# Kernel tuning notes

Hardware: AMD Instinct MI355X
Metric: run time of the kernel (lower is better)

The kernel has to match this reference:

```python
import jax, jax.numpy as jnp
import numpy as np

B, F, C, NS, P, N = 256, 2048, 16384, 65536, 8, 32
T, W_BU, W_H, P_MARGIN, N_MARGIN = 1.0, 1.0, 10.0, 0.1, 0.1


def setup_inputs() -> dict:
    key = jax.random.key(0)
    ks = jax.random.split(key, 8)
    inputs = jax.random.normal(ks[0], (B, F), jnp.float32)
    targets = jax.random.randint(ks[1], (B,), 0, C)
    # batch global indices: unique (original .item() assumes a single match)
    indexs = jax.random.permutation(ks[2], NS)[:B].astype(jnp.int64) if False else jax.random.permutation(ks[2], jnp.arange(NS))[:B]
    # positive candidates drawn from in-batch indices so they are found in `indexs`
    pos_sel = jax.random.randint(ks[3], (B, P), 0, B)
    ppairs = indexs[pos_sel]
    # negative candidates: arbitrary global indices (mostly not in batch)
    npairs = jax.random.randint(ks[4], (B, N), 0, NS)
    all_label_to_clusterid = jax.random.randint(ks[5], (NS,), 0, C)
    V = jax.random.normal(ks[6], (C, F), jnp.float32)
    V = V / jnp.linalg.norm(V, axis=1, keepdims=True)  # bank rows are L2-normalized by the update rule
    return {"inputs": inputs, "targets": targets, "ppairs": ppairs, "npairs": npairs,
            "indexs": indexs, "all_label_to_clusterid": all_label_to_clusterid, "V": V, "epoch": 1}


def _forward(inputs, targets, ppairs, npairs, indexs, all_label_to_clusterid, V, epoch):
    # Exclusive branch: logits against the memory bank (V treated as constant)
    outputs = (inputs @ V.T) * T  # [B, C]
    logp = jax.nn.log_softmax(outputs, axis=1)
    bu_loss = -jnp.mean(jnp.take_along_axis(logp, targets[:, None], axis=1))

    # ms_loss (use_prior=True, use_table=True)
    ni = inputs / jnp.linalg.norm(inputs, axis=1, keepdims=True)
    sims = ni @ ni.T          # [B, B]
    tsims = ni @ V.T          # [B, C]

    # positives found in the batch: (ppair == indexs).nonzero()
    mp = ppairs[:, :, None] == indexs[None, None, :]        # [B, P, B]
    found_p = jnp.any(mp, axis=2)
    idx_p = jnp.argmax(mp, axis=2)
    psim_b = jnp.take_along_axis(sims, idx_p, axis=1)       # [B, P]
    mask_pb = found_p & (ppairs >= 0)
    # table positive: tsims[i, target] appended if nonzero
    tp = jnp.take_along_axis(tsims, targets[:, None], axis=1)  # [B, 1]
    mask_tp = tp != 0
    psims = jnp.concatenate([psim_b, tp], axis=1)           # [B, P+1]
    pmask = jnp.concatenate([mask_pb, mask_tp], axis=1)

    # negatives found in the batch
    mn = npairs[:, :, None] == indexs[None, None, :]        # [B, N, B]
    found_n = jnp.any(mn, axis=2)
    idx_n = jnp.argmax(mn, axis=2)
    nsim_b = jnp.take_along_axis(sims, idx_n, axis=1)       # [B, N]
    mask_nb = found_n & (npairs >= 0)
    # table negative appended for EVERY npair (indent level in original): tsims[i, clusterid[npair]]
    ncid = all_label_to_clusterid[jnp.clip(npairs, 0, None)]
    tn = jnp.take_along_axis(tsims, ncid, axis=1)           # [B, N]
    mask_tn = (npairs >= 0) & (tn != 0)
    nsims = jnp.concatenate([nsim_b, tn], axis=1)           # [B, 2N]
    nmask = jnp.concatenate([mask_nb, mask_tn], axis=1)

    # thresholds: max(nsims) or -3 (+p_margin); min(psims) or 3 (-n_margin)
    p_thrd = jnp.where(jnp.any(nmask, 1), jnp.max(jnp.where(nmask, nsims, -jnp.inf), 1), -3.0) + P_MARGIN
    n_thrd = jnp.where(jnp.any(pmask, 1), jnp.min(jnp.where(pmask, psims, jnp.inf), 1), 3.0) - N_MARGIN

    hp = pmask & (psims < p_thrd[:, None])
    hn = nmask & (nsims > n_thrd[:, None]) & (nsims < 0.999999)

    hp_sum = jnp.sum(jnp.where(hp, jnp.exp(-2.0 * (psims - 0.5)), 0.0))
    hn_sum = jnp.sum(jnp.where(hn, jnp.exp(50.0 * (nsims - 0.5)), 0.0))
    hp_loss = jnp.where(jnp.any(hp), 0.5 * jnp.log1p(hp_sum), 0.0)
    hn_loss = jnp.where(jnp.any(hn), (1.0 / 50.0) * jnp.log1p(hn_sum), 0.0)
    # original builds hpsims/hnsims with torch.tensor(...), which DETACHES them
    h_loss = jax.lax.stop_gradient(hp_loss + hn_loss)

    loss = W_BU * bu_loss + W_H * h_loss
    return loss, outputs


def reference(inputs, targets, ppairs, npairs, indexs, all_label_to_clusterid, V, epoch):
    return _forward(inputs, targets, ppairs, npairs, indexs, all_label_to_clusterid, V, epoch)
```

## Files before the change

kernel.cpp:

```cpp
#include <hip/hip_runtime.h>
#include <hip/hip_bf16.h>
#include <math.h>

#define B_SZ 256
#define F_SZ 2048
#define C_SZ 16384
#define P_SZ 8
#define N_SZ 32
#define NTILE 256

typedef __bf16 bf16x8 __attribute__((ext_vector_type(8)));
typedef float f32x4 __attribute__((ext_vector_type(4)));
typedef unsigned short us8 __attribute__((ext_vector_type(8)));

typedef __attribute__((address_space(3))) unsigned int lds_u32;
typedef __attribute__((address_space(1))) const unsigned int glb_u32;

__device__ __forceinline__ unsigned short f2bf(float x) {
    union { float f; unsigned int u; } v; v.f = x;
    unsigned int r = v.u + 0x7FFFu + ((v.u >> 16) & 1u);
    return (unsigned short)(r >> 16);
}

__global__ __launch_bounds__(256) void prep_kernel(const float* __restrict__ inputs,
                                                   unsigned short* __restrict__ Abf,
                                                   float* __restrict__ norms) {
    const int row = blockIdx.x;
    const int tid = threadIdx.x;
    const float* rp = inputs + (size_t)row * F_SZ + tid * 8;
    float4 v0 = *(const float4*)(rp);
    float4 v1 = *(const float4*)(rp + 4);
    us8 o;
    o[0]=f2bf(v0.x); o[1]=f2bf(v0.y); o[2]=f2bf(v0.z); o[3]=f2bf(v0.w);
    o[4]=f2bf(v1.x); o[5]=f2bf(v1.y); o[6]=f2bf(v1.z); o[7]=f2bf(v1.w);
    *(us8*)(Abf + (size_t)row * F_SZ + tid * 8) = o;
    float ss = v0.x*v0.x + v0.y*v0.y + v0.z*v0.z + v0.w*v0.w
             + v1.x*v1.x + v1.y*v1.y + v1.z*v1.z + v1.w*v1.w;
    __shared__ float red[256];
    red[tid] = ss; __syncthreads();
    for (int s = 128; s > 0; s >>= 1) { if (tid < s) red[tid] += red[tid+s]; __syncthreads(); }
    if (tid == 0) norms[row] = sqrtf(red[0]);
}

#define BM 128
#define BN 64
#define BK 64
#define BPAD 72
#define KITERS (F_SZ / BK)

__global__ __launch_bounds__(256) void gemm_kernel(const unsigned short* __restrict__ Abf,
                                                   const float* __restrict__ V,
                                                   float* __restrict__ Cout,
                                                   float* __restrict__ pmax,
                                                   float* __restrict__ psum) {
    __shared__ unsigned short As[2][BM * BK];
    __shared__ unsigned short Bs[2][BN * BPAD];

    const int tid = threadIdx.x;
    const int lane = tid & 63;
    const int wid = tid >> 6;
    const int q = lane >> 4, l16 = lane & 15;
    const int bm0 = blockIdx.y * BM;
    const int bn0 = blockIdx.x * BN;

    f32x4 acc[2][4];
    #pragma unroll
    for (int i = 0; i < 2; i++)
        #pragma unroll
        for (int j = 0; j < 4; j++) acc[i][j] = (f32x4){0.f, 0.f, 0.f, 0.f};

    const int arow = tid >> 3;
    const int cfetch = (tid & 7) ^ (arow & 7);
    const unsigned short* AgBase = Abf + (size_t)(bm0 + arow) * F_SZ + cfetch * 8;

    const int brow = tid >> 2, bseg = tid & 3;
    const float* BgBase = V + (size_t)(bn0 + brow) * F_SZ + bseg * 16;
    unsigned short* Bsd0 = &Bs[0][brow * BPAD + bseg * 16];
    unsigned short* Bsd1 = &Bs[1][brow * BPAD + bseg * 16];

    float4 b0, b1, b2, b3;

    auto issueA = [&](int buf, int k0) {
        #pragma unroll
        for (int j = 0; j < 4; j++) {
            __builtin_amdgcn_global_load_lds(
                (glb_u32*)(AgBase + (size_t)j * 32 * F_SZ + k0),
                (lds_u32*)&As[buf][(size_t)(j * 256 + wid * 64) * 8],
                16, 0, 0);
        }
    };
    auto loadB = [&](int k0) {
        b0 = *(const float4*)(BgBase + k0);
        b1 = *(const float4*)(BgBase + k0 + 4);
        b2 = *(const float4*)(BgBase + k0 + 8);
        b3 = *(const float4*)(BgBase + k0 + 12);
    };
    auto writeB = [&](unsigned short* dst) {
        us8 w0, w1;
        w0[0]=f2bf(b0.x); w0[1]=f2bf(b0.y); w0[2]=f2bf(b0.z); w0[3]=f2bf(b0.w);
        w0[4]=f2bf(b1.x); w0[5]=f2bf(b1.y); w0[6]=f2bf(b1.z); w0[7]=f2bf(b1.w);
        w1[0]=f2bf(b2.x); w1[1]=f2bf(b2.y); w1[2]=f2bf(b2.z); w1[3]=f2bf(b2.w);
        w1[4]=f2bf(b3.x); w1[5]=f2bf(b3.y); w1[6]=f2bf(b3.z); w1[7]=f2bf(b3.w);
        *(us8*)dst = w0;
        *(us8*)(dst + 8) = w1;
    };

    issueA(0, 0);
    loadB(0);
    writeB(Bsd0);
    __syncthreads();

    for (int it = 0; it < KITERS; ++it) {
        const int cur = it & 1;
        const bool more = (it + 1) < KITERS;
        if (more) {
            issueA(cur ^ 1, (it + 1) * BK);
            loadB((it + 1) * BK);
        }
        #pragma unroll
        for (int ks = 0; ks < 2; ++ks) {
            bf16x8 af[2], bfv[4];
            #pragma unroll
            for (int mi = 0; mi < 2; ++mi) {
                const int row = wid * 32 + mi * 16 + l16;
                const int kc = ks * 4 + q;
                af[mi] = *(const bf16x8*)&As[cur][(size_t)(row * 8 + (kc ^ (row & 7))) * 8];
            }
            #pragma unroll
            for (int ni = 0; ni < 4; ++ni)
                bfv[ni] = *(const bf16x8*)&Bs[cur][(ni * 16 + l16) * BPAD + ks * 32 + q * 8];
            #pragma unroll
            for (int mi = 0; mi < 2; ++mi)
                #pragma unroll
                for (int ni = 0; ni < 4; ++ni)
                    acc[mi][ni] = __builtin_amdgcn_mfma_f32_16x16x32_bf16(af[mi], bfv[ni], acc[mi][ni], 0, 0, 0);
        }
        if (more) writeB(cur ? Bsd0 : Bsd1);
        __syncthreads();
    }

    #pragma unroll
    for (int mi = 0; mi < 2; ++mi) {
        const int r0 = bm0 + wid * 32 + mi * 16 + q * 4;
        #pragma unroll
        for (int ni = 0; ni < 4; ++ni) {
            const int c0 = bn0 + ni * 16 + l16;
            #pragma unroll
            for (int r = 0; r < 4; ++r)
                Cout[(size_t)(r0 + r) * C_SZ + c0] = acc[mi][ni][r];
        }
    }

    const int tileIdx = blockIdx.x;
    #pragma unroll
    for (int mi = 0; mi < 2; ++mi) {
        #pragma unroll
        for (int r = 0; r < 4; ++r) {
            float mloc = fmaxf(fmaxf(acc[mi][0][r], acc[mi][1][r]),
                               fmaxf(acc[mi][2][r], acc[mi][3][r]));
            #pragma unroll
            for (int off = 1; off < 16; off <<= 1)
                mloc = fmaxf(mloc, __shfl_xor(mloc, off, 64));
            float sloc = __expf(acc[mi][0][r] - mloc) + __expf(acc[mi][1][r] - mloc)
                       + __expf(acc[mi][2][r] - mloc) + __expf(acc[mi][3][r] - mloc);
            #pragma unroll
            for (int off = 1; off < 16; off <<= 1)
                sloc += __shfl_xor(sloc, off, 64);
            if (l16 == 0) {
                const int grow = bm0 + wid * 32 + mi * 16 + q * 4 + r;
                pmax[grow * NTILE + tileIdx] = mloc;
                psum[grow * NTILE + tileIdx] = sloc;
            }
        }
    }
}

__global__ __launch_bounds__(256) void softmax_combine_kernel(
    const float* __restrict__ pmax, const float* __restrict__ psum,
    const float* __restrict__ outputs, const int* __restrict__ targets,
    float* __restrict__ bu_part)
{
    const int row = blockIdx.x;
    const int tid = threadIdx.x;
    __shared__ float rm[256], rs[256];
    rm[tid] = pmax[row * NTILE + tid];
    rs[tid] = psum[row * NTILE + tid];
    __syncthreads();
    for (int s = 128; s > 0; s >>= 1) {
        if (tid < s) {
            float m1 = rm[tid], s1 = rs[tid];
            float m2 = rm[tid + s], s2 = rs[tid + s];
            float nm = fmaxf(m1, m2);
            rs[tid] = s1 * __expf(m1 - nm) + s2 * __expf(m2 - nm);
            rm[tid] = nm;
        }
        __syncthreads();
    }
    if (tid == 0) {
        float logZ = rm[0] + logf(rs[0]);
        bu_part[row] = -(outputs[(size_t)row * C_SZ + targets[row]] - logZ);
    }
}

__global__ __launch_bounds__(256) void pairs_kernel(
    const float* __restrict__ inputs, const int* __restrict__ targets,
    const int* __restrict__ ppairs, const int* __restrict__ npairs,
    const int* __restrict__ indexs, const int* __restrict__ cluster,
    const float* __restrict__ outputs, const float* __restrict__ norms,
    float* __restrict__ hp_part, float* __restrict__ hn_part,
    int* __restrict__ flag_part)
{
    const int i = blockIdx.x;
    const int tid = threadIdx.x;
    __shared__ int idxbuf[B_SZ];
    __shared__ int pj[P_SZ];
    __shared__ int nj[N_SZ];
    __shared__ float simp[P_SZ];
    __shared__ float simn[N_SZ];
    __shared__ float tnv[N_SZ];
    __shared__ float s_tp;

    idxbuf[tid] = indexs[tid];
    __syncthreads();

    const float* row = outputs + (size_t)i * C_SZ;
    const float ni_norm = norms[i];

    if (tid < P_SZ) {
        int pp = ppairs[i * P_SZ + tid];
        int f = -1;
        if (pp >= 0) for (int j = 0; j < B_SZ; j++) if (idxbuf[j] == pp) { f = j; break; }
        pj[tid] = f;
    } else if (tid < P_SZ + N_SZ) {
        int t = tid - P_SZ;
        int np = npairs[i * N_SZ + t];
        int f = -1;
        if (np >= 0) for (int j = 0; j < B_SZ; j++) if (idxbuf[j] == np) { f = j; break; }
        nj[t] = f;
        int cid = cluster[np < 0 ? 0 : np];
        tnv[t] = row[cid] / ni_norm;
    }
    if (tid == P_SZ + N_SZ) s_tp = row[targets[i]] / ni_norm;
    __syncthreads();

    const int lane = tid & 63, wv = tid >> 6;
    for (int qq = wv; qq < P_SZ + N_SZ; qq += 4) {
        int j = (qq < P_SZ) ? pj[qq] : nj[qq - P_SZ];
        float s = 0.f;
        if (j >= 0) {
            const float* xi = inputs + (size_t)i * F_SZ;
            const float* xj = inputs + (size_t)j * F_SZ;
            float d = 0.f;
            for (int k = lane; k < F_SZ; k += 64) d += xi[k] * xj[k];
            for (int off = 32; off > 0; off >>= 1) d += __shfl_down(d, off);
            s = d / (ni_norm * norms[j]);
        }
        if (lane == 0) { if (qq < P_SZ) simp[qq] = s; else simn[qq - P_SZ] = s; }
    }
    __syncthreads();

    if (tid == 0) {
        float psims[P_SZ + 1]; bool pmask[P_SZ + 1];
        for (int p = 0; p < P_SZ; p++) {
            int pp = ppairs[i * P_SZ + p];
            pmask[p] = (pj[p] >= 0) && (pp >= 0);
            psims[p] = simp[p];
        }
        psims[P_SZ] = s_tp; pmask[P_SZ] = (s_tp != 0.0f);

        float nsims[2 * N_SZ]; bool nmask[2 * N_SZ];
        for (int t = 0; t < N_SZ; t++) {
            int np = npairs[i * N_SZ + t];
            nmask[t] = (nj[t] >= 0) && (np >= 0);
            nsims[t] = simn[t];
            nsims[N_SZ + t] = tnv[t];
            nmask[N_SZ + t] = (np >= 0) && (tnv[t] != 0.0f);
        }
        bool anyp = false, anyn = false;
        float maxn = -INFINITY, minp = INFINITY;
        for (int t = 0; t < 2 * N_SZ; t++) if (nmask[t]) { anyn = true; maxn = fmaxf(maxn, nsims[t]); }
        for (int p = 0; p < P_SZ + 1; p++) if (pmask[p]) { anyp = true; minp = fminf(minp, psims[p]); }
        float p_thrd = (anyn ? maxn : -3.0f) + 0.1f;
        float n_thrd = (anyp ? minp : 3.0f) - 0.1f;
        float hps = 0.f, hns = 0.f; int fl = 0;
        for (int p = 0; p < P_SZ + 1; p++)
            if (pmask[p] && psims[p] < p_thrd) { fl |= 1; hps += expf(-2.0f * (psims[p] - 0.5f)); }
        for (int t = 0; t < 2 * N_SZ; t++)
            if (nmask[t] && nsims[t] > n_thrd && nsims[t] < 0.999999f) { fl |= 2; hns += expf(50.0f * (nsims[t] - 0.5f)); }
        hp_part[i] = hps; hn_part[i] = hns; flag_part[i] = fl;
    }
}

__global__ __launch_bounds__(256) void finalize_kernel(
    const float* __restrict__ bu_part, const float* __restrict__ hp_part,
    const float* __restrict__ hn_part, const int* __restrict__ flag_part,
    float* __restrict__ d_out)
{
    __shared__ float r1[256], r2[256], r3[256];
    __shared__ int rf[256];
    const int tid = threadIdx.x;
    r1[tid] = bu_part[tid]; r2[tid] = hp_part[tid]; r3[tid] = hn_part[tid]; rf[tid] = flag_part[tid];
    __syncthreads();
    for (int s = 128; s > 0; s >>= 1) {
        if (tid < s) { r1[tid] += r1[tid+s]; r2[tid] += r2[tid+s]; r3[tid] += r3[tid+s]; rf[tid] |= rf[tid+s]; }
        __syncthreads();
    }
    if (tid == 0) {
        float bu = r1[0] / (float)B_SZ;
        float hp_loss = (rf[0] & 1) ? 0.5f * log1pf(r2[0]) : 0.0f;
        float hn_loss = (rf[0] & 2) ? (1.0f / 50.0f) * log1pf(r3[0]) : 0.0f;
        d_out[0] = 1.0f * bu + 10.0f * (hp_loss + hn_loss);
    }
}

extern "C" void kernel_launch(void* const* d_in, const int* in_sizes, int n_in,
                              void* d_out, int out_size, void* d_ws, size_t ws_size,
                              hipStream_t stream) {
    const float* inputs  = (const float*)d_in[0];
    const int*   targets = (const int*)d_in[1];
    const int*   ppairs  = (const int*)d_in[2];
    const int*   npairs  = (const int*)d_in[3];
    const int*   indexs  = (const int*)d_in[4];
    const int*   cluster = (const int*)d_in[5];
    const float* V       = (const float*)d_in[6];
    float* out = (float*)d_out;

    char* ws = (char*)d_ws;
    unsigned short* Abf = (unsigned short*)ws;
    float* norms   = (float*)(ws + (size_t)B_SZ * F_SZ * 2);
    float* bu_part = norms + B_SZ;
    float* hp_part = bu_part + B_SZ;
    float* hn_part = hp_part + B_SZ;
    int*   flag_part = (int*)(hn_part + B_SZ);
    float* pmax = (float*)(flag_part + B_SZ);
    float* psum = pmax + (size_t)B_SZ * NTILE;

    prep_kernel<<<B_SZ, 256, 0, stream>>>(inputs, Abf, norms);
    gemm_kernel<<<dim3(C_SZ / BN, B_SZ / BM), 256, 0, stream>>>(Abf, V, out + 1, pmax, psum);
    softmax_combine_kernel<<<B_SZ, 256, 0, stream>>>(pmax, psum, out + 1, targets, bu_part);
    pairs_kernel<<<B_SZ, 256, 0, stream>>>(inputs, targets, ppairs, npairs, indexs,
                                           cluster, out + 1, norms,
                                           hp_part, hn_part, flag_part);
    finalize_kernel<<<1, 256, 0, stream>>>(bu_part, hp_part, hn_part, flag_part, out);
}
```

Measured before the change: 302.8 us.

## Cover all batch rows per block so each V tile is read once

The GEMM now uses 1024-thread blocks spanning all 256 batch rows with a 64-column slice of V. Each V element is therefore loaded and converted to bf16 once instead of once per row-block. K-step drops to 32 and each wave computes a 32x32 sub-tile, with partial softmax stats emitted per 32-column half (512 tiles). The combine kernel reduces two entries per thread. The trade-off is more barriers per unit of MFMA work and fewer blocks in the grid, which lowers latency hiding.

```diff
diff --git a/kernel.cpp b/kernel.cpp
--- a/kernel.cpp
+++ b/kernel.cpp
@@ -7,11 +7,12 @@
 #define C_SZ 16384
 #define P_SZ 8
 #define N_SZ 32
-#define NTILE 256
+#define NTILE 512
 
 typedef __bf16 bf16x8 __attribute__((ext_vector_type(8)));
 typedef float f32x4 __attribute__((ext_vector_type(4)));
 typedef unsigned short us8 __attribute__((ext_vector_type(8)));
+typedef unsigned short us4 __attribute__((ext_vector_type(4)));
 
 typedef __attribute__((address_space(3))) unsigned int lds_u32;
 typedef __attribute__((address_space(1))) const unsigned int glb_u32;
@@ -42,67 +43,56 @@
     if (tid == 0) norms[row] = sqrtf(red[0]);
 }
 
-#define BM 128
+#define BM 256
 #define BN 64
-#define BK 64
-#define BPAD 72
+#define BK 32
+#define BPAD 40
 #define KITERS (F_SZ / BK)
 
-__global__ __launch_bounds__(256) void gemm_kernel(const unsigned short* __restrict__ Abf,
-                                                   const float* __restrict__ V,
-                                                   float* __restrict__ Cout,
-                                                   float* __restrict__ pmax,
-                                                   float* __restrict__ psum) {
-    __shared__ unsigned short As[2][BM * BK];
+__global__ __launch_bounds__(1024) void gemm_kernel(const unsigned short* __restrict__ Abf,
+                                                    const float* __restrict__ V,
+                                                    float* __restrict__ Cout,
+                                                    float* __restrict__ pmax,
+                                                    float* __restrict__ psum) {
+    __shared__ unsigned short As[2][4 * 256 * 8];
     __shared__ unsigned short Bs[2][BN * BPAD];
 
     const int tid = threadIdx.x;
     const int lane = tid & 63;
     const int wid = tid >> 6;
+    const int wrow = wid & 7, wcol = wid >> 3;
     const int q = lane >> 4, l16 = lane & 15;
-    const int bm0 = blockIdx.y * BM;
     const int bn0 = blockIdx.x * BN;
 
-    f32x4 acc[2][4];
+    f32x4 acc[2][2];
     #pragma unroll
     for (int i = 0; i < 2; i++)
         #pragma unroll
-        for (int j = 0; j < 4; j++) acc[i][j] = (f32x4){0.f, 0.f, 0.f, 0.f};
-
-    const int arow = tid >> 3;
-    const int cfetch = (tid & 7) ^ (arow & 7);
-    const unsigned short* AgBase = Abf + (size_t)(bm0 + arow) * F_SZ + cfetch * 8;
-
-    const int brow = tid >> 2, bseg = tid & 3;
-    const float* BgBase = V + (size_t)(bn0 + brow) * F_SZ + bseg * 16;
-    unsigned short* Bsd0 = &Bs[0][brow * BPAD + bseg * 16];
-    unsigned short* Bsd1 = &Bs[1][brow * BPAD + bseg * 16];
-
-    float4 b0, b1, b2, b3;
+        for (int j = 0; j < 2; j++) acc[i][j] = (f32x4){0.f, 0.f, 0.f, 0.f};
+
+    const int arow = tid & 255, achk = tid >> 8;
+    const unsigned short* AgBase = Abf + (size_t)arow * F_SZ + achk * 8;
+
+    const int brow = tid >> 3, bseg = tid & 7;
+    const float* BgBase = V + (size_t)(bn0 + brow) * F_SZ + bseg * 4;
+    unsigned short* Bsd0 = &Bs[0][brow * BPAD + bseg * 4];
+    unsigned short* Bsd1 = &Bs[1][brow * BPAD + bseg * 4];
+
+    float4 bv;
 
     auto issueA = [&](int buf, int k0) {
-        #pragma unroll
-        for (int j = 0; j < 4; j++) {
-            __builtin_amdgcn_global_load_lds(
-                (glb_u32*)(AgBase + (size_t)j * 32 * F_SZ + k0),
-                (lds_u32*)&As[buf][(size_t)(j * 256 + wid * 64) * 8],
-                16, 0, 0);
-        }
+        __builtin_amdgcn_global_load_lds((glb_u32*)(AgBase + k0),
+                                         (lds_u32*)&As[buf][(size_t)tid * 8], 16, 0, 0);
     };
     auto loadB = [&](int k0) {
-        b0 = *(const float4*)(BgBase + k0);
-        b1 = *(const float4*)(BgBase + k0 + 4);
-        b2 = *(const float4*)(BgBase + k0 + 8);
-        b3 = *(const float4*)(BgBase + k0 + 12);
+        if (tid < 512) bv = *(const float4*)(BgBase + k0);
     };
     auto writeB = [&](unsigned short* dst) {
-        us8 w0, w1;
-        w0[0]=f2bf(b0.x); w0[1]=f2bf(b0.y); w0[2]=f2bf(b0.z); w0[3]=f2bf(b0.w);
-        w0[4]=f2bf(b1.x); w0[5]=f2bf(b1.y); w0[6]=f2bf(b1.z); w0[7]=f2bf(b1.w);
-        w1[0]=f2bf(b2.x); w1[1]=f2bf(b2.y); w1[2]=f2bf(b2.z); w1[3]=f2bf(b2.w);
-        w1[4]=f2bf(b3.x); w1[5]=f2bf(b3.y); w1[6]=f2bf(b3.z); w1[7]=f2bf(b3.w);
-        *(us8*)dst = w0;
-        *(us8*)(dst + 8) = w1;
+        if (tid < 512) {
+            us4 w;
+            w[0]=f2bf(bv.x); w[1]=f2bf(bv.y); w[2]=f2bf(bv.z); w[3]=f2bf(bv.w);
+            *(us4*)dst = w;
+        }
     };
 
     issueA(0, 0);
@@ -117,57 +107,53 @@
             issueA(cur ^ 1, (it + 1) * BK);
             loadB((it + 1) * BK);
         }
-        #pragma unroll
-        for (int ks = 0; ks < 2; ++ks) {
-            bf16x8 af[2], bfv[4];
+        bf16x8 af[2], bfv[2];
+        #pragma unroll
+        for (int mi = 0; mi < 2; ++mi) {
+            const int row = wrow * 32 + mi * 16 + l16;
+            af[mi] = *(const bf16x8*)&As[cur][(size_t)(q * 256 + row) * 8];
+        }
+        #pragma unroll
+        for (int ni = 0; ni < 2; ++ni) {
+            const int col = wcol * 32 + ni * 16 + l16;
+            bfv[ni] = *(const bf16x8*)&Bs[cur][col * BPAD + q * 8];
+        }
+        #pragma unroll
+        for (int mi = 0; mi < 2; ++mi)
             #pragma unroll
-            for (int mi = 0; mi < 2; ++mi) {
-                const int row = wid * 32 + mi * 16 + l16;
-                const int kc = ks * 4 + q;
-                af[mi] = *(const bf16x8*)&As[cur][(size_t)(row * 8 + (kc ^ (row & 7))) * 8];
-            }
-            #pragma unroll
-            for (int ni = 0; ni < 4; ++ni)
-                bfv[ni] = *(const bf16x8*)&Bs[cur][(ni * 16 + l16) * BPAD + ks * 32 + q * 8];
-            #pragma unroll
-            for (int mi = 0; mi < 2; ++mi)
-                #pragma unroll
-                for (int ni = 0; ni < 4; ++ni)
-                    acc[mi][ni] = __builtin_amdgcn_mfma_f32_16x16x32_bf16(af[mi], bfv[ni], acc[mi][ni], 0, 0, 0);
-        }
+            for (int ni = 0; ni < 2; ++ni)
+                acc[mi][ni] = __builtin_amdgcn_mfma_f32_16x16x32_bf16(af[mi], bfv[ni], acc[mi][ni], 0, 0, 0);
         if (more) writeB(cur ? Bsd0 : Bsd1);
         __syncthreads();
     }
 
     #pragma unroll
     for (int mi = 0; mi < 2; ++mi) {
-        const int r0 = bm0 + wid * 32 + mi * 16 + q * 4;
-        #pragma unroll
-        for (int ni = 0; ni < 4; ++ni) {
-            const int c0 = bn0 + ni * 16 + l16;
+        const int r0 = wrow * 32 + mi * 16 + q * 4;
+        #pragma unroll
+        for (int ni = 0; ni < 2; ++ni) {
+            const int c0 = bn0 + wcol * 32 + ni * 16 + l16;
             #pragma unroll
             for (int r = 0; r < 4; ++r)
                 Cout[(size_t)(r0 + r) * C_SZ + c0] = acc[mi][ni][r];
         }
     }
 
-    const int tileIdx = blockIdx.x;
+    const int tileIdx = blockIdx.x * 2 + wcol;
     #pragma unroll
     for (int mi = 0; mi < 2; ++mi) {
         #pragma unroll
         for (int r = 0; r < 4; ++r) {
-            float mloc = fmaxf(fmaxf(acc[mi][0][r], acc[mi][1][r]),
-                               fmaxf(acc[mi][2][r], acc[mi][3][r]));
+            float mloc = fmaxf(acc[mi][0][r], acc[mi][1][r]);
             #pragma unroll
             for (int off = 1; off < 16; off <<= 1)
                 mloc = fmaxf(mloc, __shfl_xor(mloc, off, 64));
-            float sloc = __expf(acc[mi][0][r] - mloc) + __expf(acc[mi][1][r] - mloc)
-                       + __expf(acc[mi][2][r] - mloc) + __expf(acc[mi][3][r] - mloc);
+            float sloc = __expf(acc[mi][0][r] - mloc) + __expf(acc[mi][1][r] - mloc);
             #pragma unroll
             for (int off = 1; off < 16; off <<= 1)
                 sloc += __shfl_xor(sloc, off, 64);
             if (l16 == 0) {
-                const int grow = bm0 + wid * 32 + mi * 16 + q * 4 + r;
+                const int grow = wrow * 32 + mi * 16 + q * 4 + r;
                 pmax[grow * NTILE + tileIdx] = mloc;
                 psum[grow * NTILE + tileIdx] = sloc;
             }
@@ -183,16 +169,19 @@
     const int row = blockIdx.x;
     const int tid = threadIdx.x;
     __shared__ float rm[256], rs[256];
-    rm[tid] = pmax[row * NTILE + tid];
-    rs[tid] = psum[row * NTILE + tid];
+    float m1 = pmax[row * NTILE + tid],       s1 = psum[row * NTILE + tid];
+    float m2 = pmax[row * NTILE + tid + 256], s2 = psum[row * NTILE + tid + 256];
+    float nm = fmaxf(m1, m2);
+    rm[tid] = nm;
+    rs[tid] = s1 * __expf(m1 - nm) + s2 * __expf(m2 - nm);
     __syncthreads();
     for (int s = 128; s > 0; s >>= 1) {
         if (tid < s) {
-            float m1 = rm[tid], s1 = rs[tid];
-            float m2 = rm[tid + s], s2 = rs[tid + s];
-            float nm = fmaxf(m1, m2);
-            rs[tid] = s1 * __expf(m1 - nm) + s2 * __expf(m2 - nm);
-            rm[tid] = nm;
+            float a = rm[tid], sa = rs[tid];
+            float b = rm[tid + s], sb = rs[tid + s];
+            float nn = fmaxf(a, b);
+            rs[tid] = sa * __expf(a - nn) + sb * __expf(b - nn);
+            rm[tid] = nn;
         }
         __syncthreads();
     }
@@ -336,7 +325,7 @@
     float* psum = pmax + (size_t)B_SZ * NTILE;
 
     prep_kernel<<<B_SZ, 256, 0, stream>>>(inputs, Abf, norms);
-    gemm_kernel<<<dim3(C_SZ / BN, B_SZ / BM), 256, 0, stream>>>(Abf, V, out + 1, pmax, psum);
+    gemm_kernel<<<dim3(C_SZ / BN, 1), 1024, 0, stream>>>(Abf, V, out + 1, pmax, psum);
     softmax_combine_kernel<<<B_SZ, 256, 0, stream>>>(pmax, psum, out + 1, targets, bu_part);
     pairs_kernel<<<B_SZ, 256, 0, stream>>>(inputs, targets, ppairs, npairs, indexs,
                                            cluster, out + 1, norms,
```

Measured after the change: 337.1 us. 11.3% more time.

## Triple-buffer A tiles with explicit waitcnts, 2x2 warp layout, and swizzled block order

Applied to the files above, without the earlier changes.

The GEMM gets a three-stage LDS ring for A tiles, issued two iterations ahead, with explicit vmcnt/lgkmcnt waits and a raw s_barrier in place of __syncthreads. This is meant to hide global latency better. Warps move from a 4x1 to a 2x2 layout, which changes per-warp fragment reuse. Grid is now a 1D index that places both M-halves of each V slab next to each other for L2 reuse. Per-block softmax partials are merged in LDS before being written. The hand-coded waitcnt values rely on the compiler's instruction ordering and could be fragile, and launch_bounds(256,2) may limit registers.

```diff
diff --git a/kernel.cpp b/kernel.cpp
--- a/kernel.cpp
+++ b/kernel.cpp
@@ -15,6 +15,10 @@
 
 typedef __attribute__((address_space(3))) unsigned int lds_u32;
 typedef __attribute__((address_space(1))) const unsigned int glb_u32;
+
+#define WAITCNT_VM4   0x0F74
+#define WAITCNT_VM0   0x0F70
+#define WAITCNT_LGKM0 0xC07F
 
 __device__ __forceinline__ unsigned short f2bf(float x) {
     union { float f; unsigned int u; } v; v.f = x;
@@ -48,44 +52,49 @@
 #define BPAD 72
 #define KITERS (F_SZ / BK)
 
-__global__ __launch_bounds__(256) void gemm_kernel(const unsigned short* __restrict__ Abf,
-                                                   const float* __restrict__ V,
-                                                   float* __restrict__ Cout,
-                                                   float* __restrict__ pmax,
-                                                   float* __restrict__ psum) {
-    __shared__ unsigned short As[2][BM * BK];
+__global__ __launch_bounds__(256, 2) void gemm_kernel(const unsigned short* __restrict__ Abf,
+                                                      const float* __restrict__ V,
+                                                      float* __restrict__ Cout,
+                                                      float* __restrict__ pmax,
+                                                      float* __restrict__ psum) {
+    __shared__ unsigned short As[3][BM * BK];
     __shared__ unsigned short Bs[2][BN * BPAD];
+    __shared__ float sm[BM * 2], ss2[BM * 2];
 
     const int tid = threadIdx.x;
     const int lane = tid & 63;
     const int wid = tid >> 6;
+    const int wm = wid >> 1, wn = wid & 1;
     const int q = lane >> 4, l16 = lane & 15;
-    const int bm0 = blockIdx.y * BM;
-    const int bn0 = blockIdx.x * BN;
-
-    f32x4 acc[2][4];
+
+    const int bid = blockIdx.x;
+    const int mhalf = (bid >> 3) & 1;
+    const int slab  = (bid & 7) | ((bid >> 4) << 3);
+    const int bm0 = mhalf * BM;
+    const int bn0 = slab * BN;
+
+    f32x4 acc[4][2];
     #pragma unroll
-    for (int i = 0; i < 2; i++)
-        #pragma unroll
-        for (int j = 0; j < 4; j++) acc[i][j] = (f32x4){0.f, 0.f, 0.f, 0.f};
+    for (int i = 0; i < 4; i++)
+        #pragma unroll
+        for (int j = 0; j < 2; j++) acc[i][j] = (f32x4){0.f, 0.f, 0.f, 0.f};
 
     const int arow = tid >> 3;
-    const int cfetch = (tid & 7) ^ (arow & 7);
-    const unsigned short* AgBase = Abf + (size_t)(bm0 + arow) * F_SZ + cfetch * 8;
-
-    const int brow = tid >> 2, bseg = tid & 3;
-    const float* BgBase = V + (size_t)(bn0 + brow) * F_SZ + bseg * 16;
-    unsigned short* Bsd0 = &Bs[0][brow * BPAD + bseg * 16];
-    unsigned short* Bsd1 = &Bs[1][brow * BPAD + bseg * 16];
+    const int akc = (tid & 7) ^ (arow & 7);
+    const unsigned short* AgBase = Abf + (size_t)(bm0 + arow) * F_SZ + akc * 8;
+
+    const int bcol = tid >> 2, bseg = tid & 3;
+    const float* BgBase = V + (size_t)(bn0 + bcol) * F_SZ + bseg * 16;
+    const int bsoff = bcol * BPAD + bseg * 16;
 
     float4 b0, b1, b2, b3;
 
-    auto issueA = [&](int buf, int k0) {
-        #pragma unroll
-        for (int j = 0; j < 4; j++) {
+    auto issueA = [&](int ring, int k0) {
+        #pragma unroll
+        for (int j = 0; j < 4; ++j) {
             __builtin_amdgcn_global_load_lds(
                 (glb_u32*)(AgBase + (size_t)j * 32 * F_SZ + k0),
-                (lds_u32*)&As[buf][(size_t)(j * 256 + wid * 64) * 8],
+                (lds_u32*)&As[ring][(j * 256 + wid * 64) * 8],
                 16, 0, 0);
         }
     };
@@ -95,83 +104,102 @@
         b2 = *(const float4*)(BgBase + k0 + 8);
         b3 = *(const float4*)(BgBase + k0 + 12);
     };
-    auto writeB = [&](unsigned short* dst) {
+    auto writeB = [&](int buf) {
         us8 w0, w1;
         w0[0]=f2bf(b0.x); w0[1]=f2bf(b0.y); w0[2]=f2bf(b0.z); w0[3]=f2bf(b0.w);
         w0[4]=f2bf(b1.x); w0[5]=f2bf(b1.y); w0[6]=f2bf(b1.z); w0[7]=f2bf(b1.w);
         w1[0]=f2bf(b2.x); w1[1]=f2bf(b2.y); w1[2]=f2bf(b2.z); w1[3]=f2bf(b2.w);
         w1[4]=f2bf(b3.x); w1[5]=f2bf(b3.y); w1[6]=f2bf(b3.z); w1[7]=f2bf(b3.w);
-        *(us8*)dst = w0;
-        *(us8*)(dst + 8) = w1;
+        *(us8*)&Bs[buf][bsoff] = w0;
+        *(us8*)&Bs[buf][bsoff + 8] = w1;
     };
+    auto compute = [&](int ring, int buf) {
+        #pragma unroll
+        for (int ks = 0; ks < 2; ++ks) {
+            bf16x8 af[4], bfv[2];
+            const int kc = ks * 4 + q;
+            #pragma unroll
+            for (int mi = 0; mi < 4; ++mi) {
+                const int row = wm * 64 + mi * 16 + l16;
+                af[mi] = *(const bf16x8*)&As[ring][row * 64 + (kc ^ (row & 7)) * 8];
+            }
+            #pragma unroll
+            for (int ni = 0; ni < 2; ++ni) {
+                const int col = wn * 32 + ni * 16 + l16;
+                bfv[ni] = *(const bf16x8*)&Bs[buf][col * BPAD + ks * 32 + q * 8];
+            }
+            #pragma unroll
+            for (int mi = 0; mi < 4; ++mi)
+                #pragma unroll
+                for (int ni = 0; ni < 2; ++ni)
+                    acc[mi][ni] = __builtin_amdgcn_mfma_f32_16x16x32_bf16(af[mi], bfv[ni], acc[mi][ni], 0, 0, 0);
+        }
+    };
 
     issueA(0, 0);
+    issueA(1, BK);
     loadB(0);
-    writeB(Bsd0);
-    __syncthreads();
-
+    __builtin_amdgcn_s_waitcnt(WAITCNT_VM0);
+    writeB(0);
+    __syncthreads();
+
+    int cur = 0;
+    int nxt2 = 2;
+    #pragma unroll 1
     for (int it = 0; it < KITERS; ++it) {
-        const int cur = it & 1;
-        const bool more = (it + 1) < KITERS;
-        if (more) {
-            issueA(cur ^ 1, (it + 1) * BK);
-            loadB((it + 1) * BK);
-        }
-        #pragma unroll
-        for (int ks = 0; ks < 2; ++ks) {
-            bf16x8 af[2], bfv[4];
-            #pragma unroll
-            for (int mi = 0; mi < 2; ++mi) {
-                const int row = wid * 32 + mi * 16 + l16;
-                const int kc = ks * 4 + q;
-                af[mi] = *(const bf16x8*)&As[cur][(size_t)(row * 8 + (kc ^ (row & 7))) * 8];
-            }
-            #pragma unroll
-            for (int ni = 0; ni < 4; ++ni)
-                bfv[ni] = *(const bf16x8*)&Bs[cur][(ni * 16 + l16) * BPAD + ks * 32 + q * 8];
-            #pragma unroll
-            for (int mi = 0; mi < 2; ++mi)
-                #pragma unroll
-                for (int ni = 0; ni < 4; ++ni)
-                    acc[mi][ni] = __builtin_amdgcn_mfma_f32_16x16x32_bf16(af[mi], bfv[ni], acc[mi][ni], 0, 0, 0);
-        }
-        if (more) writeB(cur ? Bsd0 : Bsd1);
-        __syncthreads();
+        if (it + 1 < KITERS) loadB((it + 1) * BK);
+        if (it + 2 < KITERS) issueA(nxt2, (it + 2) * BK);
+        compute(cur, it & 1);
+        if (it + 2 < KITERS)      __builtin_amdgcn_s_waitcnt(WAITCNT_VM4);
+        else if (it + 1 < KITERS) __builtin_amdgcn_s_waitcnt(WAITCNT_VM0);
+        if (it + 1 < KITERS) {
+            writeB((it + 1) & 1);
+            __builtin_amdgcn_s_waitcnt(WAITCNT_LGKM0);
+            __builtin_amdgcn_s_barrier();
+        }
+        cur  = (cur == 2) ? 0 : cur + 1;
+        nxt2 = (nxt2 == 2) ? 0 : nxt2 + 1;
     }
 
     #pragma unroll
-    for (int mi = 0; mi < 2; ++mi) {
-        const int r0 = bm0 + wid * 32 + mi * 16 + q * 4;
-        #pragma unroll
-        for (int ni = 0; ni < 4; ++ni) {
-            const int c0 = bn0 + ni * 16 + l16;
+    for (int mi = 0; mi < 4; ++mi) {
+        const int r0 = bm0 + wm * 64 + mi * 16 + q * 4;
+        #pragma unroll
+        for (int ni = 0; ni < 2; ++ni) {
+            const int c0 = bn0 + wn * 32 + ni * 16 + l16;
             #pragma unroll
             for (int r = 0; r < 4; ++r)
                 Cout[(size_t)(r0 + r) * C_SZ + c0] = acc[mi][ni][r];
         }
     }
 
-    const int tileIdx = blockIdx.x;
     #pragma unroll
-    for (int mi = 0; mi < 2; ++mi) {
+    for (int mi = 0; mi < 4; ++mi) {
         #pragma unroll
         for (int r = 0; r < 4; ++r) {
-            float mloc = fmaxf(fmaxf(acc[mi][0][r], acc[mi][1][r]),
-                               fmaxf(acc[mi][2][r], acc[mi][3][r]));
+            float mloc = fmaxf(acc[mi][0][r], acc[mi][1][r]);
             #pragma unroll
             for (int off = 1; off < 16; off <<= 1)
                 mloc = fmaxf(mloc, __shfl_xor(mloc, off, 64));
-            float sloc = __expf(acc[mi][0][r] - mloc) + __expf(acc[mi][1][r] - mloc)
-                       + __expf(acc[mi][2][r] - mloc) + __expf(acc[mi][3][r] - mloc);
+            float sloc = __expf(acc[mi][0][r] - mloc) + __expf(acc[mi][1][r] - mloc);
             #pragma unroll
             for (int off = 1; off < 16; off <<= 1)
                 sloc += __shfl_xor(sloc, off, 64);
             if (l16 == 0) {
-                const int grow = bm0 + wid * 32 + mi * 16 + q * 4 + r;
-                pmax[grow * NTILE + tileIdx] = mloc;
-                psum[grow * NTILE + tileIdx] = sloc;
+                const int lrow = wm * 64 + mi * 16 + q * 4 + r;
+                sm[lrow * 2 + wn] = mloc;
+                ss2[lrow * 2 + wn] = sloc;
             }
         }
+    }
+    __syncthreads();
+    if (tid < BM) {
+        float m1 = sm[tid * 2], s1 = ss2[tid * 2];
+        float m2 = sm[tid * 2 + 1], s2 = ss2[tid * 2 + 1];
+        float nm = fmaxf(m1, m2);
+        float s = s1 * __expf(m1 - nm) + s2 * __expf(m2 - nm);
+        pmax[(bm0 + tid) * NTILE + slab] = nm;
+        psum[(bm0 + tid) * NTILE + slab] = s;
     }
 }
 
@@ -188,11 +216,11 @@
     __syncthreads();
     for (int s = 128; s > 0; s >>= 1) {
         if (tid < s) {
-            float m1 = rm[tid], s1 = rs[tid];
-            float m2 = rm[tid + s], s2 = rs[tid + s];
-            float nm = fmaxf(m1, m2);
-            rs[tid] = s1 * __expf(m1 - nm) + s2 * __expf(m2 - nm);
-            rm[tid] = nm;
+            float a = rm[tid], sa = rs[tid];
+            float b = rm[tid + s], sb = rs[tid + s];
+            float nn = fmaxf(a, b);
+            rs[tid] = sa * __expf(a - nn) + sb * __expf(b - nn);
+            rm[tid] = nn;
         }
         __syncthreads();
     }
@@ -336,7 +364,7 @@
     float* psum = pmax + (size_t)B_SZ * NTILE;
 
     prep_kernel<<<B_SZ, 256, 0, stream>>>(inputs, Abf, norms);
-    gemm_kernel<<<dim3(C_SZ / BN, B_SZ / BM), 256, 0, stream>>>(Abf, V, out + 1, pmax, psum);
+    gemm_kernel<<<512, 256, 0, stream>>>(Abf, V, out + 1, pmax, psum);
     softmax_combine_kernel<<<B_SZ, 256, 0, stream>>>(pmax, psum, out + 1, targets, bu_part);
     pairs_kernel<<<B_SZ, 256, 0, stream>>>(inputs, targets, ppairs, npairs, indexs,
                                            cluster, out + 1, norms,
```

After: 300.6 us. About the same (-0.7%).
